# Optimization experiments

Measured on AMD Instinct MI355X. Metric: run time of the kernel, lower is better.

## Reference

```python
import jax, jax.numpy as jnp
import numpy as np
import math

GROUPS = 32
EPS = 1e-5
N_HEADS = 8  # channels=512 / num_head_channels=64


def group_norm(x, w, b):
    # x: [B, C, T]; GroupNorm over (channels-in-group, T)
    B, C, T = x.shape
    xg = x.reshape(B, GROUPS, C // GROUPS * T)
    mu = xg.mean(axis=-1, keepdims=True)
    var = xg.var(axis=-1, keepdims=True)
    xn = ((xg - mu) * jax.lax.rsqrt(var + EPS)).reshape(B, C, T)
    return xn * w[None, :, None] + b[None, :, None]


def setup_inputs() -> dict:
    key = jax.random.key(0)
    ks = jax.random.split(key, 7)
    C = 512
    return {
        "x": jax.random.normal(ks[0], (8, C, 32, 32), dtype=jnp.float32),
        "norm_w": jax.random.normal(ks[1], (C,), dtype=jnp.float32),
        "norm_b": jax.random.normal(ks[2], (C,), dtype=jnp.float32),
        "qkv_w": jax.random.normal(ks[3], (3 * C, C), dtype=jnp.float32) * 0.02,
        "qkv_b": jax.random.normal(ks[4], (3 * C,), dtype=jnp.float32) * 0.02,
        "proj_w": jax.random.normal(ks[5], (C, C), dtype=jnp.float32) * 0.02,
        "proj_b": jax.random.normal(ks[6], (C,), dtype=jnp.float32) * 0.02,
    }


def reference(x, norm_w, norm_b, qkv_w, qkv_b, proj_w, proj_b):
    b, c, H, W = x.shape
    T = H * W
    xf = x.reshape(b, c, T)
    xn = group_norm(xf, norm_w, norm_b)
    # 1x1 conv1d == channel matmul: [3C, C] x [B, C, T] -> [B, 3C, T]
    qkv = jnp.einsum('oc,bct->bot', qkv_w, xn) + qkv_b[None, :, None]
    ch = c // N_HEADS
    qkv = qkv.reshape(b * N_HEADS, 3 * ch, T)
    q, k, v = qkv[:, :ch], qkv[:, ch:2 * ch], qkv[:, 2 * ch:]
    scale = 1.0 / math.sqrt(math.sqrt(ch))
    # [BH, T, T] score matrix (explicit, as in the original)
    weight = jnp.einsum('bct,bcs->bts', q * scale, k * scale)
    weight = jax.nn.softmax(weight.astype(jnp.float32), axis=-1).astype(qkv.dtype)
    a = jnp.einsum('bts,bcs->bct', weight, v).reshape(b, c, T)
    hout = jnp.einsum('oc,bct->bot', proj_w, a) + proj_b[None, :, None]
    return (xf + hout).reshape(b, c, H, W)
```

## Files before the change

kernel.cpp:

```cpp
#include <hip/hip_runtime.h>
#include <math.h>

typedef float f32x4_t __attribute__((ext_vector_type(4)));
typedef short bf16x8_t __attribute__((ext_vector_type(8)));

#define B_   8
#define C_   512
#define T_   1024
#define NH_  8
#define CH_  64
#define EPSF 1e-5f

#define MFMA16(a, b, c) __builtin_amdgcn_mfma_f32_16x16x32_bf16((a), (b), (c), 0, 0, 0)

#define GLD16(gp, lp) __builtin_amdgcn_global_load_lds( \
    (const __attribute__((address_space(1))) unsigned int*)(gp), \
    (__attribute__((address_space(3))) unsigned int*)(lp), 16, 0, 0)

__device__ __forceinline__ unsigned short f2bf(float f) {
  union { float f; unsigned u; } v; v.f = f;
  unsigned r = v.u + 0x7FFFu + ((v.u >> 16) & 1u);
  return (unsigned short)(r >> 16);
}

__global__ __launch_bounds__(256) void prep_gn_kernel(
    const float* __restrict__ x, const float* __restrict__ w,
    const float* __restrict__ bvec, unsigned short* __restrict__ xnT,
    const float* __restrict__ qw_f, const float* __restrict__ pw_f,
    unsigned short* __restrict__ qw, unsigned short* __restrict__ pw)
{
  __shared__ __align__(16) float xs[16 * 1024];
  __shared__ float rs_[4], r2_[4];
  __shared__ float mu_s, rsig_s;

  int tid = threadIdx.x;
  if (blockIdx.x >= 256) {
    int idx = (blockIdx.x - 256) * 256 + tid;
    const int N1 = 1536 * 512 / 4;
    const int N2 = 512 * 512 / 4;
    if (idx < N1) {
      float4 v = ((const float4*)qw_f)[idx];
      uint2 o;
      o.x = (unsigned)f2bf(v.x) | ((unsigned)f2bf(v.y) << 16);
      o.y = (unsigned)f2bf(v.z) | ((unsigned)f2bf(v.w) << 16);
      ((uint2*)qw)[idx] = o;
    } else if (idx < N1 + N2) {
      int j = idx - N1;
      float4 v = ((const float4*)pw_f)[j];
      uint2 o;
      o.x = (unsigned)f2bf(v.x) | ((unsigned)f2bf(v.y) << 16);
      o.y = (unsigned)f2bf(v.z) | ((unsigned)f2bf(v.w) << 16);
      ((uint2*)pw)[j] = o;
    }
    return;
  }

  int blk = blockIdx.x;
  int b = blk >> 5, g = blk & 31;
  const float* xp = x + ((size_t)(b * C_ + g * 16)) * T_;
  const int N = 16 * T_;

  float s = 0.f, s2 = 0.f;
  for (int i = tid * 4; i < N; i += 256 * 4) {
    float4 v = *(const float4*)(xp + i);
    *(float4*)&xs[i] = v;
    s  += v.x + v.y + v.z + v.w;
    s2 += v.x * v.x + v.y * v.y + v.z * v.z + v.w * v.w;
  }
  for (int off = 32; off; off >>= 1) {
    s  += __shfl_down(s,  off, 64);
    s2 += __shfl_down(s2, off, 64);
  }
  int wid = tid >> 6, lane = tid & 63;
  if (lane == 0) { rs_[wid] = s; r2_[wid] = s2; }
  __syncthreads();
  if (tid == 0) {
    float ts = rs_[0] + rs_[1] + rs_[2] + rs_[3];
    float t2 = r2_[0] + r2_[1] + r2_[2] + r2_[3];
    float mu = ts / (float)N;
    float var = t2 / (float)N - mu * mu;
    mu_s = mu;
    rsig_s = rsqrtf(var + EPSF);
  }
  __syncthreads();
  float mu = mu_s, rs = rsig_s;

  float wl[16], bl[16];
  for (int c = 0; c < 16; ++c) { wl[c] = w[g * 16 + c]; bl[c] = bvec[g * 16 + c]; }

  for (int t = tid; t < T_; t += 256) {
    unsigned short buf[16] __attribute__((aligned(16)));
    for (int c = 0; c < 16; ++c) {
      float val = xs[c * T_ + t];
      buf[c] = f2bf((val - mu) * rs * wl[c] + bl[c]);
    }
    unsigned short* dst = xnT + ((size_t)b * T_ + t) * C_ + g * 16;
    *(uint4*)dst       = *(uint4*)buf;
    *(uint4*)(dst + 8) = *(uint4*)(buf + 8);
  }
}

__global__ __launch_bounds__(256) void gemm_qkv_kernel(
    const unsigned short* __restrict__ W, const unsigned short* __restrict__ xnT,
    const float* __restrict__ bias,
    unsigned short* __restrict__ q_t, unsigned short* __restrict__ k_t,
    unsigned short* __restrict__ v_c)
{
  int b = blockIdx.z;
  int m0 = blockIdx.y * 128, n0 = blockIdx.x * 128;
  int tid = threadIdx.x;
  int w = tid >> 6, lane = tid & 63, quad = lane >> 4, lr = lane & 15;
  int wm = w >> 1, wn = w & 1;

  __shared__ __align__(16) unsigned short Asl[2][128][32];
  __shared__ __align__(16) unsigned short Bsl[2][128][32];

  f32x4_t acc[4][4];
  for (int i = 0; i < 4; ++i)
    for (int j = 0; j < 4; ++j) acc[i][j] = (f32x4_t){0.f, 0.f, 0.f, 0.f};

  int ur = tid >> 2, uk = (tid & 3) * 8;
  const unsigned short* Ap = W + (size_t)(m0 + ur) * C_ + uk;
  const unsigned short* Bp = xnT + ((size_t)b * T_ + n0 + ur) * C_ + uk;

#define STAGE_QKV(buf, k0)                                        \
  do {                                                            \
    GLD16(Ap + (k0),            &Asl[buf][w * 16][0]);            \
    GLD16(Ap + 64 * C_ + (k0),  &Asl[buf][64 + w * 16][0]);       \
    GLD16(Bp + (k0),            &Bsl[buf][w * 16][0]);            \
    GLD16(Bp + 64 * C_ + (k0),  &Bsl[buf][64 + w * 16][0]);       \
  } while (0)

  STAGE_QKV(0, 0);
  __syncthreads();

  int cur = 0;
  for (int k0 = 0; k0 < C_; k0 += 32) {
    if (k0 + 32 < C_) STAGE_QKV(cur ^ 1, k0 + 32);
    bf16x8_t af[4], bfv[4];
    for (int i = 0; i < 4; ++i) af[i]  = *(bf16x8_t*)&Asl[cur][wm * 64 + i * 16 + lr][quad * 8];
    for (int j = 0; j < 4; ++j) bfv[j] = *(bf16x8_t*)&Bsl[cur][wn * 64 + j * 16 + lr][quad * 8];
    for (int i = 0; i < 4; ++i)
      for (int j = 0; j < 4; ++j)
        acc[i][j] = MFMA16(af[i], bfv[j], acc[i][j]);
    __syncthreads();
    cur ^= 1;
  }
#undef STAGE_QKV

  for (int i = 0; i < 4; ++i) {
    int ob = m0 + wm * 64 + i * 16 + quad * 4;
    int h = ob / 192, r0 = ob % 192;
    for (int j = 0; j < 4; ++j) {
      int t = n0 + wn * 64 + j * 16 + lr;
      if (r0 < 128) {
        unsigned short pk[4] __attribute__((aligned(8)));
      #pragma unroll
        for (int r = 0; r < 4; ++r) pk[r] = f2bf(acc[i][j][r] + bias[ob + r]);
        unsigned short* base = (r0 < 64) ? q_t : k_t;
        int chn = (r0 < 64) ? r0 : r0 - 64;
        *(uint2*)&base[((size_t)(b * NH_ + h) * T_ + t) * CH_ + chn] = *(uint2*)pk;
      } else {
      #pragma unroll
        for (int r = 0; r < 4; ++r) {
          float vv = acc[i][j][r] + bias[ob + r];
          v_c[((size_t)(b * NH_ + h) * CH_ + (r0 - 128 + r)) * T_ + t] = f2bf(vv);
        }
      }
    }
  }
}

__global__ __launch_bounds__(256) void attn_kernel(
    const unsigned short* __restrict__ q_t, const unsigned short* __restrict__ k_t,
    const unsigned short* __restrict__ v_c, unsigned short* __restrict__ a_t)
{
  int bh = blockIdx.x;
  int t0 = blockIdx.y * 128;
  int tid = threadIdx.x;
  int w = tid >> 6, lane = tid & 63, quad = lane >> 4, lr = lane & 15;

  __shared__ __align__(16) unsigned short k_s[64][72];
  __shared__ __align__(16) unsigned short p_s[128][72];

  int r0 = tid >> 3, c0 = (tid & 7) * 8;

  bf16x8_t bq[2][2];
#pragma unroll
  for (int rb = 0; rb < 2; ++rb)
#pragma unroll
    for (int kk = 0; kk < 2; ++kk)
      bq[rb][kk] = *(const bf16x8_t*)
          &q_t[((size_t)bh * T_ + t0 + w * 32 + rb * 16 + lr) * CH_ + kk * 32 + quad * 8];

  uint4 kr0 = *(const uint4*)&k_t[((size_t)bh * T_ + r0) * CH_ + c0];
  uint4 kr1 = *(const uint4*)&k_t[((size_t)bh * T_ + r0 + 32) * CH_ + c0];

  const unsigned short* vbase = v_c + ((size_t)bh * CH_ + lr) * T_ + quad * 8;

  f32x4_t o_acc[2][4];
#pragma unroll
  for (int rb = 0; rb < 2; ++rb)
    for (int j = 0; j < 4; ++j) o_acc[rb][j] = (f32x4_t){0.f, 0.f, 0.f, 0.f};
  float l_sum[2] = {0.f, 0.f};

  const float SCL = 0.18033688f;
  const float MSH = 11.541560f;

  for (int s0 = 0; s0 < T_; s0 += 64) {
    __syncthreads();
    *(uint4*)&k_s[r0][c0]      = kr0;
    *(uint4*)&k_s[r0 + 32][c0] = kr1;
    __syncthreads();
    if (s0 + 64 < T_) {
      kr0 = *(const uint4*)&k_t[((size_t)bh * T_ + s0 + 64 + r0) * CH_ + c0];
      kr1 = *(const uint4*)&k_t[((size_t)bh * T_ + s0 + 96 + r0) * CH_ + c0];
    }

    bf16x8_t bvv[4][2];
#pragma unroll
    for (int j = 0; j < 4; ++j)
#pragma unroll
      for (int kk = 0; kk < 2; ++kk)
        bvv[j][kk] = *(const bf16x8_t*)(vbase + (size_t)j * 16 * T_ + s0 + kk * 32);

#pragma unroll
    for (int j = 0; j < 4; ++j) {
      bf16x8_t ak0 = *(bf16x8_t*)&k_s[j * 16 + lr][quad * 8];
      bf16x8_t ak1 = *(bf16x8_t*)&k_s[j * 16 + lr][32 + quad * 8];
      f32x4_t a0 = (f32x4_t){0.f, 0.f, 0.f, 0.f};
      f32x4_t a1 = (f32x4_t){0.f, 0.f, 0.f, 0.f};
      a0 = MFMA16(ak0, bq[0][0], a0);
      a0 = MFMA16(ak1, bq[0][1], a0);
      a1 = MFMA16(ak0, bq[1][0], a1);
      a1 = MFMA16(ak1, bq[1][1], a1);
#pragma unroll
      for (int rb = 0; rb < 2; ++rb) {
        const f32x4_t& av = rb ? a1 : a0;
        unsigned u[4];
        float rsum = 0.f;
#pragma unroll
        for (int r = 0; r < 4; ++r) {
          union { float f; unsigned v; } cv;
          cv.f = __builtin_amdgcn_exp2f(av[r] * SCL - MSH);
          u[r] = cv.v & 0xFFFF0000u;
          union { unsigned v; float f; } rf; rf.v = u[r];
          rsum += rf.f;
        }
        uint2 pk;
        pk.x = (u[0] >> 16) | u[1];
        pk.y = (u[2] >> 16) | u[3];
        *(uint2*)&p_s[w * 32 + rb * 16 + lr][j * 16 + quad * 4] = pk;
        l_sum[rb] += rsum;
      }
    }
#pragma unroll
    for (int rb = 0; rb < 2; ++rb) {
    }

    bf16x8_t ap[2][2];
#pragma unroll
    for (int rb = 0; rb < 2; ++rb) {
      ap[rb][0] = *(bf16x8_t*)&p_s[w * 32 + rb * 16 + lr][quad * 8];
      ap[rb][1] = *(bf16x8_t*)&p_s[w * 32 + rb * 16 + lr][32 + quad * 8];
    }

    __builtin_amdgcn_s_setprio(1);
#pragma unroll
    for (int j = 0; j < 4; ++j)
#pragma unroll
      for (int kk = 0; kk < 2; ++kk) {
        o_acc[0][j] = MFMA16(ap[0][kk], bvv[j][kk], o_acc[0][j]);
        o_acc[1][j] = MFMA16(ap[1][kk], bvv[j][kk], o_acc[1][j]);
      }
    __builtin_amdgcn_s_setprio(0);
  }

#pragma unroll
  for (int rb = 0; rb < 2; ++rb) {
    l_sum[rb] += __shfl_xor(l_sum[rb], 16, 64);
    l_sum[rb] += __shfl_xor(l_sum[rb], 32, 64);
  }

#pragma unroll
  for (int rb = 0; rb < 2; ++rb) {
#pragma unroll
    for (int r = 0; r < 4; ++r) {
      float lv = __shfl(l_sum[rb], quad * 4 + r, 64);
      float inv = 1.f / lv;
#pragma unroll
      for (int j = 0; j < 4; ++j)
        p_s[w * 32 + rb * 16 + quad * 4 + r][j * 16 + lr] = f2bf(o_acc[rb][j][r] * inv);
    }
  }
  __syncthreads();
#pragma unroll
  for (int cch = 0; cch < 4; ++cch)
    *(uint4*)&a_t[((size_t)bh * T_ + t0 + r0 + 32 * cch) * CH_ + c0] =
        *(uint4*)&p_s[r0 + 32 * cch][c0];
}

__global__ __launch_bounds__(256) void gemm_proj_kernel(
    const unsigned short* __restrict__ W, const unsigned short* __restrict__ a_t,
    const float* __restrict__ bias, const float* __restrict__ xres,
    float* __restrict__ out)
{
  int b = blockIdx.z;
  int m0 = blockIdx.y * 128, n0 = blockIdx.x * 128;
  int tid = threadIdx.x;
  int w = tid >> 6, lane = tid & 63, quad = lane >> 4, lr = lane & 15;
  int wm = w >> 1, wn = w & 1;

  __shared__ __align__(16) unsigned short Asl[2][128][32];
  __shared__ __align__(16) unsigned short Bsl[2][128][32];

  f32x4_t acc[4][4];
  for (int i = 0; i < 4; ++i)
    for (int j = 0; j < 4; ++j) acc[i][j] = (f32x4_t){0.f, 0.f, 0.f, 0.f};

  int ur = tid >> 2, uk = (tid & 3) * 8;
  const unsigned short* Ap = W + (size_t)(m0 + ur) * C_ + uk;

#define STAGE_PROJ(buf, k0)                                                   \
  do {                                                                        \
    const unsigned short* Bp = a_t +                                          \
        ((size_t)(b * NH_ + ((k0) >> 6)) * T_ + n0 + ur) * CH_ + ((k0) & 63) + uk; \
    GLD16(Ap + (k0),           &Asl[buf][w * 16][0]);                         \
    GLD16(Ap + 64 * C_ + (k0), &Asl[buf][64 + w * 16][0]);                    \
    GLD16(Bp,                  &Bsl[buf][w * 16][0]);                         \
    GLD16(Bp + 64 * CH_,       &Bsl[buf][64 + w * 16][0]);                    \
  } while (0)

  STAGE_PROJ(0, 0);
  __syncthreads();

  int cur = 0;
  for (int k0 = 0; k0 < C_; k0 += 32) {
    if (k0 + 32 < C_) STAGE_PROJ(cur ^ 1, k0 + 32);
    bf16x8_t af[4], bfv[4];
    for (int i = 0; i < 4; ++i) af[i]  = *(bf16x8_t*)&Asl[cur][wm * 64 + i * 16 + lr][quad * 8];
    for (int j = 0; j < 4; ++j) bfv[j] = *(bf16x8_t*)&Bsl[cur][wn * 64 + j * 16 + lr][quad * 8];
    for (int i = 0; i < 4; ++i)
      for (int j = 0; j < 4; ++j)
        acc[i][j] = MFMA16(af[i], bfv[j], acc[i][j]);
    __syncthreads();
    cur ^= 1;
  }
#undef STAGE_PROJ

  for (int i = 0; i < 4; ++i) {
    int ob = m0 + wm * 64 + i * 16 + quad * 4;
    for (int j = 0; j < 4; ++j) {
      int t = n0 + wn * 64 + j * 16 + lr;
    #pragma unroll
      for (int r = 0; r < 4; ++r) {
        size_t idx = ((size_t)(b * C_ + ob + r)) * T_ + t;
        out[idx] = acc[i][j][r] + bias[ob + r] + xres[idx];
      }
    }
  }
}

extern "C" void kernel_launch(void* const* d_in, const int* in_sizes, int n_in,
                              void* d_out, int out_size, void* d_ws, size_t ws_size,
                              hipStream_t stream)
{
  const float* x      = (const float*)d_in[0];
  const float* norm_w = (const float*)d_in[1];
  const float* norm_b = (const float*)d_in[2];
  const float* qkv_w  = (const float*)d_in[3];
  const float* qkv_b  = (const float*)d_in[4];
  const float* proj_w = (const float*)d_in[5];
  const float* proj_b = (const float*)d_in[6];
  float* out = (float*)d_out;

  char* ws = (char*)d_ws;
  unsigned short* qw  = (unsigned short*)ws;
  unsigned short* pw  = (unsigned short*)(ws + 1572864);
  unsigned short* xnT = (unsigned short*)(ws + 2097152);
  unsigned short* q_t = (unsigned short*)(ws + 10485760);
  unsigned short* k_t = (unsigned short*)(ws + 18874368);
  unsigned short* v_c = (unsigned short*)(ws + 27262976);
  unsigned short* a_t = (unsigned short*)(ws + 35651584);

  prep_gn_kernel<<<dim3(256 + 1024), dim3(256), 0, stream>>>(
      x, norm_w, norm_b, xnT, qkv_w, proj_w, qw, pw);

  gemm_qkv_kernel<<<dim3(T_ / 128, 1536 / 128, B_), dim3(256), 0, stream>>>(
      qw, xnT, qkv_b, q_t, k_t, v_c);

  attn_kernel<<<dim3(B_ * NH_, T_ / 128), dim3(256), 0, stream>>>(q_t, k_t, v_c, a_t);

  gemm_proj_kernel<<<dim3(T_ / 128, C_ / 128, B_), dim3(256), 0, stream>>>(
      pw, a_t, proj_b, x, out);
}
```

Baseline: 166.9 us.

## Double attention query tile to 256 and stage V through shared memory

The attention kernel now handles 256 query rows per block instead of 128, so each wave computes four 16-row blocks. That halves how many times K and V are re-read per head. V tiles are now loaded cooperatively into LDS with register prefetch, alongside K, instead of each wave loading V fragments directly from global memory. The trade-off is half as many blocks (about one per CU), more accumulator registers and more LDS per block, which may reduce latency hiding.

```diff
diff --git a/kernel.cpp b/kernel.cpp
--- a/kernel.cpp
+++ b/kernel.cpp
@@ -176,33 +176,34 @@
     const unsigned short* __restrict__ v_c, unsigned short* __restrict__ a_t)
 {
   int bh = blockIdx.x;
-  int t0 = blockIdx.y * 128;
+  int t0 = blockIdx.y * 256;
   int tid = threadIdx.x;
   int w = tid >> 6, lane = tid & 63, quad = lane >> 4, lr = lane & 15;
 
   __shared__ __align__(16) unsigned short k_s[64][72];
-  __shared__ __align__(16) unsigned short p_s[128][72];
+  __shared__ __align__(16) unsigned short v_s[64][72];
+  __shared__ __align__(16) unsigned short p_s[256][72];
 
   int r0 = tid >> 3, c0 = (tid & 7) * 8;
 
-  bf16x8_t bq[2][2];
-#pragma unroll
-  for (int rb = 0; rb < 2; ++rb)
+  bf16x8_t bq[4][2];
+#pragma unroll
+  for (int rb = 0; rb < 4; ++rb)
 #pragma unroll
     for (int kk = 0; kk < 2; ++kk)
       bq[rb][kk] = *(const bf16x8_t*)
-          &q_t[((size_t)bh * T_ + t0 + w * 32 + rb * 16 + lr) * CH_ + kk * 32 + quad * 8];
+          &q_t[((size_t)bh * T_ + t0 + w * 64 + rb * 16 + lr) * CH_ + kk * 32 + quad * 8];
 
   uint4 kr0 = *(const uint4*)&k_t[((size_t)bh * T_ + r0) * CH_ + c0];
   uint4 kr1 = *(const uint4*)&k_t[((size_t)bh * T_ + r0 + 32) * CH_ + c0];
-
-  const unsigned short* vbase = v_c + ((size_t)bh * CH_ + lr) * T_ + quad * 8;
-
-  f32x4_t o_acc[2][4];
-#pragma unroll
-  for (int rb = 0; rb < 2; ++rb)
+  uint4 vr0 = *(const uint4*)&v_c[((size_t)bh * CH_ + r0) * T_ + c0];
+  uint4 vr1 = *(const uint4*)&v_c[((size_t)bh * CH_ + r0 + 32) * T_ + c0];
+
+  f32x4_t o_acc[4][4];
+#pragma unroll
+  for (int rb = 0; rb < 4; ++rb)
     for (int j = 0; j < 4; ++j) o_acc[rb][j] = (f32x4_t){0.f, 0.f, 0.f, 0.f};
-  float l_sum[2] = {0.f, 0.f};
+  float l_sum[4] = {0.f, 0.f, 0.f, 0.f};
 
   const float SCL = 0.18033688f;
   const float MSH = 11.541560f;
@@ -211,38 +212,36 @@
     __syncthreads();
     *(uint4*)&k_s[r0][c0]      = kr0;
     *(uint4*)&k_s[r0 + 32][c0] = kr1;
-    __syncthreads();
+    *(uint4*)&v_s[r0][c0]      = vr0;
+    *(uint4*)&v_s[r0 + 32][c0] = vr1;
     if (s0 + 64 < T_) {
       kr0 = *(const uint4*)&k_t[((size_t)bh * T_ + s0 + 64 + r0) * CH_ + c0];
       kr1 = *(const uint4*)&k_t[((size_t)bh * T_ + s0 + 96 + r0) * CH_ + c0];
-    }
-
-    bf16x8_t bvv[4][2];
-#pragma unroll
-    for (int j = 0; j < 4; ++j)
-#pragma unroll
-      for (int kk = 0; kk < 2; ++kk)
-        bvv[j][kk] = *(const bf16x8_t*)(vbase + (size_t)j * 16 * T_ + s0 + kk * 32);
+      vr0 = *(const uint4*)&v_c[((size_t)bh * CH_ + r0) * T_ + s0 + 64 + c0];
+      vr1 = *(const uint4*)&v_c[((size_t)bh * CH_ + r0 + 32) * T_ + s0 + 64 + c0];
+    }
+    __syncthreads();
 
 #pragma unroll
     for (int j = 0; j < 4; ++j) {
       bf16x8_t ak0 = *(bf16x8_t*)&k_s[j * 16 + lr][quad * 8];
       bf16x8_t ak1 = *(bf16x8_t*)&k_s[j * 16 + lr][32 + quad * 8];
-      f32x4_t a0 = (f32x4_t){0.f, 0.f, 0.f, 0.f};
-      f32x4_t a1 = (f32x4_t){0.f, 0.f, 0.f, 0.f};
-      a0 = MFMA16(ak0, bq[0][0], a0);
-      a0 = MFMA16(ak1, bq[0][1], a0);
-      a1 = MFMA16(ak0, bq[1][0], a1);
-      a1 = MFMA16(ak1, bq[1][1], a1);
-#pragma unroll
-      for (int rb = 0; rb < 2; ++rb) {
-        const f32x4_t& av = rb ? a1 : a0;
+      f32x4_t av[4];
+#pragma unroll
+      for (int rb = 0; rb < 4; ++rb) {
+        f32x4_t a = (f32x4_t){0.f, 0.f, 0.f, 0.f};
+        a = MFMA16(ak0, bq[rb][0], a);
+        a = MFMA16(ak1, bq[rb][1], a);
+        av[rb] = a;
+      }
+#pragma unroll
+      for (int rb = 0; rb < 4; ++rb) {
         unsigned u[4];
         float rsum = 0.f;
 #pragma unroll
         for (int r = 0; r < 4; ++r) {
           union { float f; unsigned v; } cv;
-          cv.f = __builtin_amdgcn_exp2f(av[r] * SCL - MSH);
+          cv.f = __builtin_amdgcn_exp2f(av[rb][r] * SCL - MSH);
           u[r] = cv.v & 0xFFFF0000u;
           union { unsigned v; float f; } rf; rf.v = u[r];
           rsum += rf.f;
@@ -250,52 +249,52 @@
         uint2 pk;
         pk.x = (u[0] >> 16) | u[1];
         pk.y = (u[2] >> 16) | u[3];
-        *(uint2*)&p_s[w * 32 + rb * 16 + lr][j * 16 + quad * 4] = pk;
+        *(uint2*)&p_s[w * 64 + rb * 16 + lr][j * 16 + quad * 4] = pk;
         l_sum[rb] += rsum;
       }
     }
-#pragma unroll
-    for (int rb = 0; rb < 2; ++rb) {
-    }
-
-    bf16x8_t ap[2][2];
-#pragma unroll
-    for (int rb = 0; rb < 2; ++rb) {
-      ap[rb][0] = *(bf16x8_t*)&p_s[w * 32 + rb * 16 + lr][quad * 8];
-      ap[rb][1] = *(bf16x8_t*)&p_s[w * 32 + rb * 16 + lr][32 + quad * 8];
+
+    bf16x8_t ap[4][2];
+#pragma unroll
+    for (int rb = 0; rb < 4; ++rb) {
+      ap[rb][0] = *(bf16x8_t*)&p_s[w * 64 + rb * 16 + lr][quad * 8];
+      ap[rb][1] = *(bf16x8_t*)&p_s[w * 64 + rb * 16 + lr][32 + quad * 8];
     }
 
     __builtin_amdgcn_s_setprio(1);
 #pragma unroll
-    for (int j = 0; j < 4; ++j)
-#pragma unroll
-      for (int kk = 0; kk < 2; ++kk) {
-        o_acc[0][j] = MFMA16(ap[0][kk], bvv[j][kk], o_acc[0][j]);
-        o_acc[1][j] = MFMA16(ap[1][kk], bvv[j][kk], o_acc[1][j]);
-      }
+    for (int j = 0; j < 4; ++j) {
+      bf16x8_t bv0 = *(bf16x8_t*)&v_s[j * 16 + lr][quad * 8];
+      bf16x8_t bv1 = *(bf16x8_t*)&v_s[j * 16 + lr][32 + quad * 8];
+#pragma unroll
+      for (int rb = 0; rb < 4; ++rb) {
+        o_acc[rb][j] = MFMA16(ap[rb][0], bv0, o_acc[rb][j]);
+        o_acc[rb][j] = MFMA16(ap[rb][1], bv1, o_acc[rb][j]);
+      }
+    }
     __builtin_amdgcn_s_setprio(0);
   }
 
 #pragma unroll
-  for (int rb = 0; rb < 2; ++rb) {
+  for (int rb = 0; rb < 4; ++rb) {
     l_sum[rb] += __shfl_xor(l_sum[rb], 16, 64);
     l_sum[rb] += __shfl_xor(l_sum[rb], 32, 64);
   }
 
 #pragma unroll
-  for (int rb = 0; rb < 2; ++rb) {
+  for (int rb = 0; rb < 4; ++rb) {
 #pragma unroll
     for (int r = 0; r < 4; ++r) {
       float lv = __shfl(l_sum[rb], quad * 4 + r, 64);
       float inv = 1.f / lv;
 #pragma unroll
       for (int j = 0; j < 4; ++j)
-        p_s[w * 32 + rb * 16 + quad * 4 + r][j * 16 + lr] = f2bf(o_acc[rb][j][r] * inv);
-    }
-  }
-  __syncthreads();
-#pragma unroll
-  for (int cch = 0; cch < 4; ++cch)
+        p_s[w * 64 + rb * 16 + quad * 4 + r][j * 16 + lr] = f2bf(o_acc[rb][j][r] * inv);
+    }
+  }
+  __syncthreads();
+#pragma unroll
+  for (int cch = 0; cch < 8; ++cch)
     *(uint4*)&a_t[((size_t)bh * T_ + t0 + r0 + 32 * cch) * CH_ + c0] =
         *(uint4*)&p_s[r0 + 32 * cch][c0];
 }
@@ -389,7 +388,7 @@
   gemm_qkv_kernel<<<dim3(T_ / 128, 1536 / 128, B_), dim3(256), 0, stream>>>(
       qw, xnT, qkv_b, q_t, k_t, v_c);
 
-  attn_kernel<<<dim3(B_ * NH_, T_ / 128), dim3(256), 0, stream>>>(q_t, k_t, v_c, a_t);
+  attn_kernel<<<dim3(B_ * NH_, T_ / 256), dim3(256), 0, stream>>>(q_t, k_t, v_c, a_t);
 
   gemm_proj_kernel<<<dim3(T_ / 128, C_ / 128, B_), dim3(256), 0, stream>>>(
       pw, a_t, proj_b, x, out);
```

New measurement: 164.6 us. About the same (-1.4%).
